# Optimization experiments

Hardware: AMD Instinct MI355X
Metric: run time of the kernel (lower is better)

The kernel has to match this reference:

```python
import jax, jax.numpy as jnp
import numpy as np

C = 512

def _xavier(key, shape, gain=1.0):
    fan_in, fan_out = shape[1], shape[0]
    a = gain * np.sqrt(6.0 / (fan_in + fan_out))
    return jax.random.uniform(key, shape, jnp.float32, -a, a)

def setup_inputs() -> dict:
    key = jax.random.key(0)
    ks = jax.random.split(key, 5)
    x = jax.random.normal(ks[0], (32, C, 32, 32), jnp.float32)
    # 1x1 conv weights as [out_ch, in_ch]; biases zero-init per module
    Wq = _xavier(ks[1], (C, C))
    Wk = _xavier(ks[2], (C, C))
    Wv = _xavier(ks[3], (C, C))
    Wo = _xavier(ks[4], (C, C), gain=1e-05)
    zeros = jnp.zeros((C,), jnp.float32)
    return {"x": x, "Wq": Wq, "bq": zeros, "Wk": Wk, "bk": zeros,
            "Wv": Wv, "bv": zeros, "Wo": Wo, "bo": zeros}

def _proj(x, W, b):
    # 1x1 conv: x [B,C,H,W], W [Cout,Cin] -> [B,Cout,H,W]
    return jnp.einsum('bchw,oc->bohw', x, W) + b[None, :, None, None]

def reference(x, Wq, bq, Wk, bk, Wv, bv, Wo, bo):
    B, Cc, H, W = x.shape
    q = _proj(x, Wq, bq).transpose(0, 2, 3, 1).reshape(B, H * W, Cc)  # [B,HW,C]
    k = _proj(x, Wk, bk).reshape(B, Cc, H * W)                        # [B,C,HW]
    v = _proj(x, Wv, bv).transpose(0, 2, 3, 1).reshape(B, H * W, Cc)  # [B,HW,C]
    w = jnp.einsum('bnc,bcm->bnm', q, k) * (Cc ** -0.5)               # [B,HW,HW]
    w = jax.nn.softmax(w, axis=-1)
    h = jnp.einsum('bnm,bmc->bnc', w, v)                              # [B,HW,C]
    h = h.reshape(B, H, W, Cc).transpose(0, 3, 1, 2)                  # [B,C,H,W]
    h = _proj(h, Wo, bo)
    return x + h
```

## Files before the change

### kernel.cpp

```cpp
#include <hip/hip_runtime.h>
#include <stdint.h>


#define CD 512
#define NSP 1024
#define SCALE_EXP2 0.06376339f
#define WO_SCALE 4194304.0f
#define WO_INV   2.384185791015625e-7f

using f32x4  = __attribute__((ext_vector_type(4))) float;
typedef long i64v;

__device__ __forceinline__ unsigned char f2f8(float f) {
    unsigned int r;
    asm("v_cvt_pk_fp8_f32 %0, %1, %1" : "=v"(r) : "v"(f));
    return (unsigned char)(r & 0xffu);
}
__device__ __forceinline__ unsigned int f4_to_f8x4(float a, float b, float c, float d) {
    unsigned int r = 0;
    asm("v_cvt_pk_fp8_f32 %0, %2, %3\n\t"
        "v_cvt_pk_fp8_f32 %0, %4, %5 op_sel:[0,0,1]"
        : "=v"(r) : "0"(r), "v"(a), "v"(b), "v"(c), "v"(d));
    return r;
}
__device__ __forceinline__ void gl_lds16(const void* g, void* l) {
    __builtin_amdgcn_global_load_lds(
        (const __attribute__((address_space(1))) void*)g,
        (__attribute__((address_space(3))) void*)l, 16, 0, 0);
}

__global__ __launch_bounds__(256) void prep(
    const float* __restrict__ Wq, const float* __restrict__ Wk,
    const float* __restrict__ Wv, const float* __restrict__ Wo,
    const float* __restrict__ bq, const float* __restrict__ bk,
    const float* __restrict__ x,
    unsigned char* __restrict__ w8, float* __restrict__ bqk,
    unsigned char* __restrict__ xt)
{
    const int bid = blockIdx.x;
    const int tid = threadIdx.x;
    if (bid < 4096) {
        int idx = bid * 256 + tid;
        int which = idx >> 18, off = idx & 262143;
        const float* src = which == 0 ? Wq : which == 1 ? Wk : which == 2 ? Wv : Wo;
        float v = src[off] * (which == 3 ? WO_SCALE : 1.0f);
        w8[idx] = f2f8(v);
        if (idx < 1024) bqk[idx] = (idx < 512) ? bq[idx] : bk[idx - 512];
    } else {
        __shared__ float t[32][33];
        int tb = bid - 4096;
        int n0 = (tb & 31) * 32;
        int c0 = ((tb >> 5) & 15) * 32;
        int b  = tb >> 9;
        const float* xb = x + (size_t)b * CD * NSP;
        unsigned char* xtb = xt + (size_t)b * NSP * CD;
        int tx = tid & 31, ty = tid >> 5;
        #pragma unroll
        for (int i = 0; i < 4; ++i)
            t[ty + i * 8][tx] = xb[(size_t)(c0 + ty + i * 8) * NSP + n0 + tx];
        __syncthreads();
        #pragma unroll
        for (int i = 0; i < 4; ++i)
            xtb[(size_t)(n0 + ty + i * 8) * CD + c0 + tx] = f2f8(t[tx][ty + i * 8]);
    }
}

__global__ __launch_bounds__(256)
void gemm_qkv(const unsigned char* __restrict__ Xt8,
              const unsigned char* __restrict__ W8,
              unsigned char* __restrict__ QK8,
              unsigned char* __restrict__ Vc8,
              const float* __restrict__ bqk,
              const float* __restrict__ bv)
{
    __shared__ __align__(16) unsigned char As[2][128 * 64];
    __shared__ __align__(16) unsigned char Bs[2][128 * 64];

    const int bid = blockIdx.x;
    const unsigned char *Ab, *Bb;
    unsigned char* Cp;
    const float* bias;
    int biasCol;
    if (bid < 2048) {
        int bx = bid & 7, by = bid >> 3;
        Ab = Xt8 + (size_t)by * 128 * 512;
        Bb = W8 + (size_t)bx * 128 * 512;
        Cp = QK8 + (size_t)by * 128 * 1024 + bx * 128;
        bias = bqk + bx * 128;
        biasCol = 1;
    } else {
        int t2 = bid - 2048;
        int bx = t2 & 7, by = (t2 >> 3) & 3, z = t2 >> 5;
        Ab = W8 + 524288 + (size_t)by * 128 * 512;
        Bb = Xt8 + (size_t)z * 524288 + (size_t)bx * 128 * 512;
        Cp = Vc8 + (size_t)z * 524288 + (size_t)by * 128 * 1024 + bx * 128;
        bias = bv + by * 128;
        biasCol = 0;
    }

    const int t = threadIdx.x;
    const int lane = t & 63;
    const int wave = t >> 6;
    const int wr = wave >> 1, wc = wave & 1;
    const int lr = lane & 15, lk = lane >> 4;

    f32x4 acc[4][4] = {};

    auto stage = [&](int kt, int buf) {
        int k0 = kt << 6;
        #pragma unroll
        for (int i = 0; i < 2; ++i) {
            int rb = i * 64 + wave * 16;
            int row = rb + (lane >> 2);
            int src = (lane & 3) ^ ((row >> 1) & 3);
            gl_lds16(Ab + (size_t)row * 512 + k0 + src * 16, &As[buf][rb * 64]);
            gl_lds16(Bb + (size_t)row * 512 + k0 + src * 16, &Bs[buf][rb * 64]);
        }
    };
    stage(0, 0);
    for (int kt = 0; kt < 8; ++kt) {
        int cur = kt & 1;
        if (kt < 7) {
            stage(kt + 1, cur ^ 1);
            asm volatile("s_waitcnt vmcnt(4)" ::: "memory");
        } else {
            asm volatile("s_waitcnt vmcnt(0)" ::: "memory");
        }
        __builtin_amdgcn_s_barrier();
        const unsigned char* Ac = &As[cur][0];
        const unsigned char* Bc = &Bs[cur][0];
        #pragma unroll
        for (int kk = 0; kk < 2; ++kk) {
            int c16 = kk * 2 + (lk >> 1);
            int half = (lk & 1) * 8;
            i64v af[4], bfr[4];
            #pragma unroll
            for (int f = 0; f < 4; ++f) {
                int arow = wr * 64 + f * 16 + lr;
                af[f] = *(const i64v*)&Ac[arow * 64 + ((c16 ^ ((arow >> 1) & 3)) << 4) + half];
                int brow = wc * 64 + f * 16 + lr;
                bfr[f] = *(const i64v*)&Bc[brow * 64 + ((c16 ^ ((brow >> 1) & 3)) << 4) + half];
            }
            #pragma unroll
            for (int fm = 0; fm < 4; ++fm)
                #pragma unroll
                for (int fn = 0; fn < 4; ++fn)
                    acc[fm][fn] = __builtin_amdgcn_mfma_f32_16x16x32_fp8_fp8(
                        af[fm], bfr[fn], acc[fm][fn], 0, 0, 0);
        }
        asm volatile("s_waitcnt lgkmcnt(0)" ::: "memory");
        __builtin_amdgcn_s_barrier();
    }

    #pragma unroll
    for (int fm = 0; fm < 4; ++fm) {
        #pragma unroll
        for (int fn = 0; fn < 4; ++fn) {
            int col = wc * 64 + fn * 16 + lr;
            int rowb = wr * 64 + fm * 16 + lk * 4;
            #pragma unroll
            for (int j = 0; j < 4; ++j) {
                int row = rowb + j;
                float v = acc[fm][fn][j] + (biasCol ? bias[col] : bias[row]);
                Cp[(size_t)row * 1024 + col] = f2f8(v);
            }
        }
    }
}

template<int BIAS_MODE, bool RESID, bool OUT_F32>
__global__ __launch_bounds__(256)
void gemm_bt8(const unsigned char* __restrict__ A,
              const unsigned char* __restrict__ B,
              void* __restrict__ Cv,
              const float* __restrict__ bias,
              const float* __restrict__ resid,
              int K, int lda, int ldb, int ldc,
              long sA, long sB, long sC, long sR, float alpha)
{
    __shared__ __align__(16) unsigned char As[2][128 * 64];
    __shared__ __align__(16) unsigned char Bs[2][128 * 64];

    const int z = blockIdx.z;
    const unsigned char* Ab = A + (size_t)z * sA + (size_t)blockIdx.y * 128 * lda;
    const unsigned char* Bb = B + (size_t)z * sB + (size_t)blockIdx.x * 128 * ldb;

    const int t = threadIdx.x;
    const int lane = t & 63;
    const int wave = t >> 6;
    const int wr = wave >> 1, wc = wave & 1;
    const int lr = lane & 15, lk = lane >> 4;

    f32x4 acc[4][4] = {};

    const int KT = K >> 6;
    auto stage = [&](int kt, int buf) {
        int k0 = kt << 6;
        #pragma unroll
        for (int i = 0; i < 2; ++i) {
            int rb = i * 64 + wave * 16;
            int row = rb + (lane >> 2);
            int src = (lane & 3) ^ ((row >> 1) & 3);
            gl_lds16(Ab + (size_t)row * lda + k0 + src * 16, &As[buf][rb * 64]);
            gl_lds16(Bb + (size_t)row * ldb + k0 + src * 16, &Bs[buf][rb * 64]);
        }
    };
    stage(0, 0);
    for (int kt = 0; kt < KT; ++kt) {
        int cur = kt & 1;
        if (kt + 1 < KT) {
            stage(kt + 1, cur ^ 1);
            asm volatile("s_waitcnt vmcnt(4)" ::: "memory");
        } else {
            asm volatile("s_waitcnt vmcnt(0)" ::: "memory");
        }
        __builtin_amdgcn_s_barrier();
        const unsigned char* Ac = &As[cur][0];
        const unsigned char* Bc = &Bs[cur][0];
        #pragma unroll
        for (int kk = 0; kk < 2; ++kk) {
            int c16 = kk * 2 + (lk >> 1);
            int half = (lk & 1) * 8;
            i64v af[4], bfr[4];
            #pragma unroll
            for (int f = 0; f < 4; ++f) {
                int arow = wr * 64 + f * 16 + lr;
                af[f] = *(const i64v*)&Ac[arow * 64 + ((c16 ^ ((arow >> 1) & 3)) << 4) + half];
                int brow = wc * 64 + f * 16 + lr;
                bfr[f] = *(const i64v*)&Bc[brow * 64 + ((c16 ^ ((brow >> 1) & 3)) << 4) + half];
            }
            #pragma unroll
            for (int fm = 0; fm < 4; ++fm)
                #pragma unroll
                for (int fn = 0; fn < 4; ++fn)
                    acc[fm][fn] = __builtin_amdgcn_mfma_f32_16x16x32_fp8_fp8(
                        af[fm], bfr[fn], acc[fm][fn], 0, 0, 0);
        }
        asm volatile("s_waitcnt lgkmcnt(0)" ::: "memory");
        __builtin_amdgcn_s_barrier();
    }

    const int m0 = blockIdx.y * 128;
    const int n0 = blockIdx.x * 128;
    unsigned char* C8 = (unsigned char*)Cv + (size_t)z * sC;
    float* Cf = (float*)Cv + (size_t)z * sC;
    const float* rp = RESID ? resid + (size_t)z * sR : nullptr;
    #pragma unroll
    for (int fm = 0; fm < 4; ++fm) {
        #pragma unroll
        for (int fn = 0; fn < 4; ++fn) {
            int col = n0 + wc * 64 + fn * 16 + lr;
            int rowb = m0 + wr * 64 + fm * 16 + lk * 4;
            #pragma unroll
            for (int j = 0; j < 4; ++j) {
                int row = rowb + j;
                float v = acc[fm][fn][j] * alpha;
                if (BIAS_MODE == 1) v += bias[col];
                if (BIAS_MODE == 2) v += bias[row];
                if (RESID) v += rp[(size_t)row * ldc + col];
                if (OUT_F32) Cf[(size_t)row * ldc + col] = v;
                else         C8[(size_t)row * ldc + col] = f2f8(v);
            }
        }
    }
}

__global__ __launch_bounds__(512, 2)
void flash_attn(const unsigned char* __restrict__ Q,
                const unsigned char* __restrict__ Kg,
                const unsigned char* __restrict__ Vg,
                unsigned char* __restrict__ H)
{
    __shared__ __align__(16) unsigned char Ks[2][64 * 512];
    __shared__ __align__(16) unsigned char Vs[2][512 * 64];
    __shared__ __align__(16) unsigned char Ps[2][128 * 72];
    __shared__ __align__(16) float Ls[2][128];
    __shared__ int flags[2];

    const int p = blockIdx.x;
    const int b  = ((p >> 6) << 3) + (p & 7);
    const int qt = (p >> 3) & 7;

    const int tid = threadIdx.x;
    const int w = tid >> 6, lane = tid & 63;
    const int lr = lane & 15, lk = lane >> 4;
    const int q0 = qt * 128 + w * 16;

    i64v qf[16];
    const unsigned char* qp = Q + ((size_t)b * NSP + q0 + lr) * 1024 + lk * 8;
    #pragma unroll
    for (int st = 0; st < 16; ++st) qf[st] = *(const i64v*)(qp + st * 32);

    f32x4 o[8][4] = {};
    float m = -3.0e38f, l = 0.f;

    const unsigned char* Kb = Kg + (size_t)b * NSP * 1024;
    const unsigned char* Vb = Vg + (size_t)b * CD * 1024;

    auto stageK = [&](int t, int buf) {
        int kv0 = t * 64;
        #pragma unroll
        for (int i = 0; i < 4; ++i) {
            int rb = i * 16 + w * 2;
            int row = rb + (lane >> 5);
            int src = (lane & 31) ^ (row & 7);
            gl_lds16(Kb + (size_t)(kv0 + row) * 1024 + src * 16, &Ks[buf][rb * 512]);
        }
    };
    auto stageV = [&](int t, int buf) {
        int kv0 = t * 64;
        #pragma unroll
        for (int i = 0; i < 4; ++i) {
            int cb = i * 128 + w * 16;
            int c = cb + (lane >> 2);
            int src = (lane & 3) ^ ((c >> 1) & 3);
            gl_lds16(Vb + (size_t)c * 1024 + kv0 + src * 16, &Vs[buf][cb * 64]);
        }
    };

    auto qksm = [&](int tau) {
        const int pb = tau & 1;
        const unsigned char* Kc = &Ks[pb][0];
        f32x4 s[4] = {};
        __builtin_amdgcn_s_setprio(1);
        #pragma unroll
        for (int st = 0; st < 16; ++st) {
            int c16 = st * 2 + (lk >> 1);
            int half = (lk & 1) * 8;
            #pragma unroll
            for (int kvf = 0; kvf < 4; ++kvf) {
                int row = kvf * 16 + lr;
                i64v kf = *(const i64v*)&Kc[row * 512 + ((c16 ^ (row & 7)) << 4) + half];
                s[kvf] = __builtin_amdgcn_mfma_f32_16x16x32_fp8_fp8(kf, qf[st], s[kvf], 0, 0, 0);
            }
        }
        __builtin_amdgcn_s_setprio(0);
        #pragma unroll
        for (int kvf = 0; kvf < 4; ++kvf)
            #pragma unroll
            for (int j = 0; j < 4; ++j) s[kvf][j] *= SCALE_EXP2;

        float pm = fmaxf(fmaxf(fmaxf(s[0][0], s[0][1]), fmaxf(s[0][2], s[0][3])),
                         fmaxf(fmaxf(s[1][0], s[1][1]), fmaxf(s[1][2], s[1][3])));
        pm = fmaxf(pm, fmaxf(fmaxf(fmaxf(s[2][0], s[2][1]), fmaxf(s[2][2], s[2][3])),
                             fmaxf(fmaxf(s[3][0], s[3][1]), fmaxf(s[3][2], s[3][3]))));
        pm = fmaxf(pm, __shfl_xor(pm, 16));
        pm = fmaxf(pm, __shfl_xor(pm, 32));
        bool ev = !__all(pm - m <= 8.0f);
        float mn = fmaxf(m, pm);
        float sc = ev ? exp2f(m - mn) : 1.0f;
        if (ev) { m = mn; l *= sc; }
        if (lk == 0) Ls[pb][w * 16 + lr] = sc;
        if (ev && lane == 0) flags[pb] = tau;

        float rs = 0.f;
        #pragma unroll
        for (int kvf = 0; kvf < 4; ++kvf)
            #pragma unroll
            for (int j = 0; j < 4; ++j) {
                s[kvf][j] = exp2f(s[kvf][j] - m);
                rs += s[kvf][j];
            }
        rs += __shfl_xor(rs, 16);
        rs += __shfl_xor(rs, 32);
        l += rs;

        #pragma unroll
        for (int kvf = 0; kvf < 4; ++kvf) {
            unsigned int pk = f4_to_f8x4(s[kvf][0], s[kvf][1], s[kvf][2], s[kvf][3]);
            *(unsigned int*)&Ps[pb][(w * 16 + lr) * 72 + kvf * 16 + lk * 4] = pk;
        }
    };

    if (tid == 0) { flags[0] = -1; flags[1] = -1; }
    stageK(0, 0); stageV(0, 0);
    asm volatile("s_waitcnt vmcnt(0) lgkmcnt(0)" ::: "memory");
    __builtin_amdgcn_s_barrier();
    stageK(1, 1);
    qksm(0);
    asm volatile("s_waitcnt vmcnt(0) lgkmcnt(0)" ::: "memory");
    __builtin_amdgcn_s_barrier();

    for (int t = 0; t < 16; ++t) {
        const int cur = t & 1;
        if (t < 14) stageK(t + 2, cur);
        if (t < 15) stageV(t + 1, cur ^ 1);

        if (flags[cur] == t) {
            #pragma unroll
            for (int qf2 = 0; qf2 < 8; ++qf2) {
                f32x4 scv = *(const f32x4*)&Ls[cur][qf2 * 16 + lk * 4];
                #pragma unroll
                for (int cf = 0; cf < 4; ++cf) {
                    o[qf2][cf][0] *= scv[0]; o[qf2][cf][1] *= scv[1];
                    o[qf2][cf][2] *= scv[2]; o[qf2][cf][3] *= scv[3];
                }
            }
        }
        const unsigned char* Vc = &Vs[cur][0];
        __builtin_amdgcn_s_setprio(1);
        #pragma unroll
        for (int ks = 0; ks < 2; ++ks) {
            int c16 = ks * 2 + (lk >> 1);
            int half = (lk & 1) * 8;
            i64v vfr[4];
            #pragma unroll
            for (int cf = 0; cf < 4; ++cf) {
                int c = w * 64 + cf * 16 + lr;
                vfr[cf] = *(const i64v*)&Vc[c * 64 + ((c16 ^ ((c >> 1) & 3)) << 4) + half];
            }
            #pragma unroll
            for (int qf2 = 0; qf2 < 8; ++qf2) {
                i64v pa = *(const i64v*)&Ps[cur][(qf2 * 16 + lr) * 72 + ks * 32 + lk * 8];
                #pragma unroll
                for (int cf = 0; cf < 4; ++cf)
                    o[qf2][cf] = __builtin_amdgcn_mfma_f32_16x16x32_fp8_fp8(
                        pa, vfr[cf], o[qf2][cf], 0, 0, 0);
            }
        }
        __builtin_amdgcn_s_setprio(0);

        if (t < 15) qksm(t + 1);

        asm volatile("s_waitcnt vmcnt(0) lgkmcnt(0)" ::: "memory");
        __builtin_amdgcn_s_barrier();
    }

    if (lk == 0) Ls[0][w * 16 + lr] = 1.0f / l;
    asm volatile("s_waitcnt lgkmcnt(0)" ::: "memory");
    __builtin_amdgcn_s_barrier();
    unsigned char* Hp = H + ((size_t)b * NSP + qt * 128) * CD + w * 64;
    #pragma unroll
    for (int qf2 = 0; qf2 < 8; ++qf2) {
        f32x4 li = *(const f32x4*)&Ls[0][qf2 * 16 + lk * 4];
        #pragma unroll
        for (int cf = 0; cf < 4; ++cf) {
            #pragma unroll
            for (int j = 0; j < 4; ++j)
                Hp[(size_t)(qf2 * 16 + lk * 4 + j) * CD + cf * 16 + lr] =
                    f2f8(o[qf2][cf][j] * li[j]);
        }
    }
}

extern "C" void kernel_launch(void* const* d_in, const int* in_sizes, int n_in,
                              void* d_out, int out_size, void* d_ws, size_t ws_size,
                              hipStream_t stream)
{
    const float* x  = (const float*)d_in[0];
    const float* Wq = (const float*)d_in[1];
    const float* bq = (const float*)d_in[2];
    const float* Wk = (const float*)d_in[3];
    const float* bk = (const float*)d_in[4];
    const float* Wv = (const float*)d_in[5];
    const float* bv = (const float*)d_in[6];
    const float* Wo = (const float*)d_in[7];
    const float* bo = (const float*)d_in[8];
    float* out = (float*)d_out;

    unsigned char* w = (unsigned char*)d_ws;
    unsigned char* W8  = w;
    float*         bqk = (float*)(w + 1048576);
    unsigned char* Xt8 = w + 1052672;
    unsigned char* QK8 = w + 17829888;
    unsigned char* Vc8 = w + 51384320;
    unsigned char* H8  = w + 68161536;

    prep<<<20480, 256, 0, stream>>>(Wq, Wk, Wv, Wo, bq, bk, x, W8, bqk, Xt8);

    gemm_qkv<<<3072, 256, 0, stream>>>(Xt8, W8, QK8, Vc8, bqk, bv);

    flash_attn<<<256, 512, 0, stream>>>(QK8, QK8 + 512, Vc8, H8);

    gemm_bt8<2, true, true><<<dim3(8, 4, 32), 256, 0, stream>>>(
        W8 + 786432, H8, out, bo, x, 512, 512, 512, 1024,
        0, 524288, 524288, 524288, WO_INV);
}
```

Baseline: 198.4 us.

## Fuse output projection and residual add into flash attention epilogue

The attention kernel now keeps its normalized output tile in LDS (reusing the K buffer, in a swizzled layout) and runs the Wo projection GEMM directly, adding bias and the residual before writing the fp32 output. The separate H intermediate write/read and the extra GEMM launch go away. To make this work, the PV accumulation is transposed (operands swapped) so the output lands channel-major. The epilogue adds a 512-deep GEMM per block with Wo fragments read straight from global memory, raising register pressure on a 512-thread block at 2 blocks per CU, and with only 256 blocks the projection runs at the attention kernel's occupancy.

```diff
diff --git a/kernel.cpp b/kernel.cpp
--- a/kernel.cpp
+++ b/kernel.cpp
@@ -168,108 +168,14 @@
     }
 }
 
-template<int BIAS_MODE, bool RESID, bool OUT_F32>
-__global__ __launch_bounds__(256)
-void gemm_bt8(const unsigned char* __restrict__ A,
-              const unsigned char* __restrict__ B,
-              void* __restrict__ Cv,
-              const float* __restrict__ bias,
-              const float* __restrict__ resid,
-              int K, int lda, int ldb, int ldc,
-              long sA, long sB, long sC, long sR, float alpha)
-{
-    __shared__ __align__(16) unsigned char As[2][128 * 64];
-    __shared__ __align__(16) unsigned char Bs[2][128 * 64];
-
-    const int z = blockIdx.z;
-    const unsigned char* Ab = A + (size_t)z * sA + (size_t)blockIdx.y * 128 * lda;
-    const unsigned char* Bb = B + (size_t)z * sB + (size_t)blockIdx.x * 128 * ldb;
-
-    const int t = threadIdx.x;
-    const int lane = t & 63;
-    const int wave = t >> 6;
-    const int wr = wave >> 1, wc = wave & 1;
-    const int lr = lane & 15, lk = lane >> 4;
-
-    f32x4 acc[4][4] = {};
-
-    const int KT = K >> 6;
-    auto stage = [&](int kt, int buf) {
-        int k0 = kt << 6;
-        #pragma unroll
-        for (int i = 0; i < 2; ++i) {
-            int rb = i * 64 + wave * 16;
-            int row = rb + (lane >> 2);
-            int src = (lane & 3) ^ ((row >> 1) & 3);
-            gl_lds16(Ab + (size_t)row * lda + k0 + src * 16, &As[buf][rb * 64]);
-            gl_lds16(Bb + (size_t)row * ldb + k0 + src * 16, &Bs[buf][rb * 64]);
-        }
-    };
-    stage(0, 0);
-    for (int kt = 0; kt < KT; ++kt) {
-        int cur = kt & 1;
-        if (kt + 1 < KT) {
-            stage(kt + 1, cur ^ 1);
-            asm volatile("s_waitcnt vmcnt(4)" ::: "memory");
-        } else {
-            asm volatile("s_waitcnt vmcnt(0)" ::: "memory");
-        }
-        __builtin_amdgcn_s_barrier();
-        const unsigned char* Ac = &As[cur][0];
-        const unsigned char* Bc = &Bs[cur][0];
-        #pragma unroll
-        for (int kk = 0; kk < 2; ++kk) {
-            int c16 = kk * 2 + (lk >> 1);
-            int half = (lk & 1) * 8;
-            i64v af[4], bfr[4];
-            #pragma unroll
-            for (int f = 0; f < 4; ++f) {
-                int arow = wr * 64 + f * 16 + lr;
-                af[f] = *(const i64v*)&Ac[arow * 64 + ((c16 ^ ((arow >> 1) & 3)) << 4) + half];
-                int brow = wc * 64 + f * 16 + lr;
-                bfr[f] = *(const i64v*)&Bc[brow * 64 + ((c16 ^ ((brow >> 1) & 3)) << 4) + half];
-            }
-            #pragma unroll
-            for (int fm = 0; fm < 4; ++fm)
-                #pragma unroll
-                for (int fn = 0; fn < 4; ++fn)
-                    acc[fm][fn] = __builtin_amdgcn_mfma_f32_16x16x32_fp8_fp8(
-                        af[fm], bfr[fn], acc[fm][fn], 0, 0, 0);
-        }
-        asm volatile("s_waitcnt lgkmcnt(0)" ::: "memory");
-        __builtin_amdgcn_s_barrier();
-    }
-
-    const int m0 = blockIdx.y * 128;
-    const int n0 = blockIdx.x * 128;
-    unsigned char* C8 = (unsigned char*)Cv + (size_t)z * sC;
-    float* Cf = (float*)Cv + (size_t)z * sC;
-    const float* rp = RESID ? resid + (size_t)z * sR : nullptr;
-    #pragma unroll
-    for (int fm = 0; fm < 4; ++fm) {
-        #pragma unroll
-        for (int fn = 0; fn < 4; ++fn) {
-            int col = n0 + wc * 64 + fn * 16 + lr;
-            int rowb = m0 + wr * 64 + fm * 16 + lk * 4;
-            #pragma unroll
-            for (int j = 0; j < 4; ++j) {
-                int row = rowb + j;
-                float v = acc[fm][fn][j] * alpha;
-                if (BIAS_MODE == 1) v += bias[col];
-                if (BIAS_MODE == 2) v += bias[row];
-                if (RESID) v += rp[(size_t)row * ldc + col];
-                if (OUT_F32) Cf[(size_t)row * ldc + col] = v;
-                else         C8[(size_t)row * ldc + col] = f2f8(v);
-            }
-        }
-    }
-}
-
 __global__ __launch_bounds__(512, 2)
-void flash_attn(const unsigned char* __restrict__ Q,
-                const unsigned char* __restrict__ Kg,
-                const unsigned char* __restrict__ Vg,
-                unsigned char* __restrict__ H)
+void flash_attn_out(const unsigned char* __restrict__ Q,
+                    const unsigned char* __restrict__ Kg,
+                    const unsigned char* __restrict__ Vg,
+                    const unsigned char* __restrict__ Wo8,
+                    const float* __restrict__ bo,
+                    const float* __restrict__ xg,
+                    float* __restrict__ outg)
 {
     __shared__ __align__(16) unsigned char Ks[2][64 * 512];
     __shared__ __align__(16) unsigned char Vs[2][512 * 64];
@@ -291,7 +197,7 @@
     #pragma unroll
     for (int st = 0; st < 16; ++st) qf[st] = *(const i64v*)(qp + st * 32);
 
-    f32x4 o[8][4] = {};
+    f32x4 o[4][8] = {};
     float m = -3.0e38f, l = 0.f;
 
     const unsigned char* Kb = Kg + (size_t)b * NSP * 1024;
@@ -389,11 +295,11 @@
         if (flags[cur] == t) {
             #pragma unroll
             for (int qf2 = 0; qf2 < 8; ++qf2) {
-                f32x4 scv = *(const f32x4*)&Ls[cur][qf2 * 16 + lk * 4];
+                float scq = Ls[cur][qf2 * 16 + lr];
                 #pragma unroll
                 for (int cf = 0; cf < 4; ++cf) {
-                    o[qf2][cf][0] *= scv[0]; o[qf2][cf][1] *= scv[1];
-                    o[qf2][cf][2] *= scv[2]; o[qf2][cf][3] *= scv[3];
+                    o[cf][qf2][0] *= scq; o[cf][qf2][1] *= scq;
+                    o[cf][qf2][2] *= scq; o[cf][qf2][3] *= scq;
                 }
             }
         }
@@ -414,8 +320,8 @@
                 i64v pa = *(const i64v*)&Ps[cur][(qf2 * 16 + lr) * 72 + ks * 32 + lk * 8];
                 #pragma unroll
                 for (int cf = 0; cf < 4; ++cf)
-                    o[qf2][cf] = __builtin_amdgcn_mfma_f32_16x16x32_fp8_fp8(
-                        pa, vfr[cf], o[qf2][cf], 0, 0, 0);
+                    o[cf][qf2] = __builtin_amdgcn_mfma_f32_16x16x32_fp8_fp8(
+                        vfr[cf], pa, o[cf][qf2], 0, 0, 0);
             }
         }
         __builtin_amdgcn_s_setprio(0);
@@ -429,16 +335,61 @@
     if (lk == 0) Ls[0][w * 16 + lr] = 1.0f / l;
     asm volatile("s_waitcnt lgkmcnt(0)" ::: "memory");
     __builtin_amdgcn_s_barrier();
-    unsigned char* Hp = H + ((size_t)b * NSP + qt * 128) * CD + w * 64;
+    unsigned char* Hs = &Ks[0][0];
     #pragma unroll
     for (int qf2 = 0; qf2 < 8; ++qf2) {
-        f32x4 li = *(const f32x4*)&Ls[0][qf2 * 16 + lk * 4];
+        float inv = Ls[0][qf2 * 16 + lr];
+        int qrow = qf2 * 16 + lr;
         #pragma unroll
         for (int cf = 0; cf < 4; ++cf) {
-            #pragma unroll
-            for (int j = 0; j < 4; ++j)
-                Hp[(size_t)(qf2 * 16 + lk * 4 + j) * CD + cf * 16 + lr] =
-                    f2f8(o[qf2][cf][j] * li[j]);
+            unsigned int pk = f4_to_f8x4(o[cf][qf2][0] * inv, o[cf][qf2][1] * inv,
+                                         o[cf][qf2][2] * inv, o[cf][qf2][3] * inv);
+            int chunk = (w * 4 + cf) ^ (lr & 7);
+            *(unsigned int*)&Hs[qrow * 512 + chunk * 16 + lk * 4] = pk;
+        }
+    }
+    asm volatile("s_waitcnt lgkmcnt(0)" ::: "memory");
+    __builtin_amdgcn_s_barrier();
+
+    f32x4 acc[4][8] = {};
+    #pragma unroll
+    for (int kst = 0; kst < 16; ++kst) {
+        int c16 = kst * 2 + (lk >> 1);
+        int half = (lk & 1) * 8;
+        i64v af[4];
+        #pragma unroll
+        for (int mf = 0; mf < 4; ++mf)
+            af[mf] = *(const i64v*)(Wo8 + (size_t)(w * 64 + mf * 16 + lr) * 512
+                                    + kst * 32 + lk * 8);
+        i64v bfr[8];
+        #pragma unroll
+        for (int nf = 0; nf < 8; ++nf)
+            bfr[nf] = *(const i64v*)&Hs[(nf * 16 + lr) * 512
+                                        + ((c16 ^ (lr & 7)) << 4) + half];
+        #pragma unroll
+        for (int mf = 0; mf < 4; ++mf)
+            #pragma unroll
+            for (int nf = 0; nf < 8; ++nf)
+                acc[mf][nf] = __builtin_amdgcn_mfma_f32_16x16x32_fp8_fp8(
+                    af[mf], bfr[nf], acc[mf][nf], 0, 0, 0);
+    }
+
+    const size_t bb = (size_t)b * CD * NSP;
+    float* op = outg + bb;
+    const float* xp = xg + bb;
+    const int colbase = qt * 128;
+    #pragma unroll
+    for (int mf = 0; mf < 4; ++mf) {
+        #pragma unroll
+        for (int nf = 0; nf < 8; ++nf) {
+            int col = colbase + nf * 16 + lr;
+            int rowb2 = w * 64 + mf * 16 + lk * 4;
+            #pragma unroll
+            for (int j = 0; j < 4; ++j) {
+                int row = rowb2 + j;
+                op[(size_t)row * NSP + col] = acc[mf][nf][j] * WO_INV
+                    + bo[row] + xp[(size_t)row * NSP + col];
+            }
         }
     }
 }
@@ -464,15 +415,11 @@
     unsigned char* Xt8 = w + 1052672;
     unsigned char* QK8 = w + 17829888;
     unsigned char* Vc8 = w + 51384320;
-    unsigned char* H8  = w + 68161536;
 
     prep<<<20480, 256, 0, stream>>>(Wq, Wk, Wv, Wo, bq, bk, x, W8, bqk, Xt8);
 
     gemm_qkv<<<3072, 256, 0, stream>>>(Xt8, W8, QK8, Vc8, bqk, bv);
 
-    flash_attn<<<256, 512, 0, stream>>>(QK8, QK8 + 512, Vc8, H8);
-
-    gemm_bt8<2, true, true><<<dim3(8, 4, 32), 256, 0, stream>>>(
-        W8 + 786432, H8, out, bo, x, 512, 512, 512, 1024,
-        0, 524288, 524288, 524288, WO_INV);
-}
+    flash_attn_out<<<256, 512, 0, stream>>>(
+        QK8, QK8 + 512, Vc8, W8 + 786432, bo, x, out);
+}
```

New measurement: 204.4 us. 1.03x slower.
